# Optimization experiments

Hardware: AMD Instinct MI355X
Metric: run time of the kernel (lower is better)

## Reference

```python
import jax, jax.numpy as jnp
import numpy as np

BN_EPS = 1e-5


def setup_inputs() -> dict:
    key = jax.random.key(0)
    ks = jax.random.split(key, 8)
    B, S, D, H, O = 4, 25000, 128, 128, 128
    N, E = B * S, 600000
    x = jax.random.normal(ks[0], (B, S, D), dtype=jnp.float32)
    edge_index = jax.random.randint(ks[1], (2, E), 0, N)
    W1 = jax.random.normal(ks[2], (D, H), dtype=jnp.float32) * (1.0 / np.sqrt(D))
    b1 = jnp.zeros((H,), jnp.float32)
    gamma1 = jnp.ones((H,), jnp.float32)
    beta1 = jnp.zeros((H,), jnp.float32)
    W2 = jax.random.normal(ks[3], (H, O), dtype=jnp.float32) * (1.0 / np.sqrt(H))
    b2 = jnp.zeros((O,), jnp.float32)
    return {"x": x, "edge_index": edge_index, "W1": W1, "b1": b1,
            "gamma1": gamma1, "beta1": beta1, "W2": W2, "b2": b2}


def _gcn_norm(edge_index, num_nodes, dtype):
    # PyG gcn_norm: add self-loops, symmetric D^-1/2 (A+I) D^-1/2 edge weights.
    row, col = edge_index
    loop = jnp.arange(num_nodes, dtype=row.dtype)
    row_f = jnp.concatenate([row, loop])
    col_f = jnp.concatenate([col, loop])
    deg = jax.ops.segment_sum(jnp.ones(row_f.shape, dtype), row_f,
                              num_segments=num_nodes)
    dis = jnp.where(deg > 0, jax.lax.rsqrt(jnp.maximum(deg, 1e-12)), 0.0)
    norm = dis[row_f] * dis[col_f]  # [E + N]
    return row_f, col_f, norm


def _gcn_conv(h, W, b, row_f, col_f, norm, num_nodes):
    hw = h @ W                       # [N, out]
    msg = hw[col_f] * norm[:, None]  # gather + scale, [E+N, out]
    out = jax.ops.segment_sum(msg, row_f, num_segments=num_nodes)
    return out + b


def reference(x, edge_index, W1, b1, gamma1, beta1, W2, b2):
    B, S, D = x.shape
    N = B * S
    h = x.reshape(N, D)
    row_f, col_f, norm = _gcn_norm(edge_index, N, h.dtype)
    # layer 1: GCNConv -> BatchNorm (batch stats) -> ReLU (dropout inactive in eval)
    h = _gcn_conv(h, W1, b1, row_f, col_f, norm, N)
    mean = jnp.mean(h, axis=0)
    var = jnp.mean(jnp.square(h - mean), axis=0)
    h = gamma1 * (h - mean) * jax.lax.rsqrt(var + BN_EPS) + beta1
    h = jax.nn.relu(h)
    # layer 2: final GCNConv
    h = _gcn_conv(h, W2, b2, row_f, col_f, norm, N)
    return h.reshape(B, S, -1)
```

## Files before the change

kernel.cpp:

```cpp
#include <hip/hip_runtime.h>

#define DIM 128
#define BN_EPS 1e-5f
#define STAT_COPIES 64

typedef short short8 __attribute__((ext_vector_type(8)));
typedef float floatx4 __attribute__((ext_vector_type(4)));

__device__ __forceinline__ unsigned short f2bf(float f) {
    unsigned int u = __builtin_bit_cast(unsigned int, f);
    u += 0x7FFFu + ((u >> 16) & 1u);
    return (unsigned short)(u >> 16);
}
__device__ __forceinline__ float bf2f(unsigned short h) {
    return __builtin_bit_cast(float, (unsigned int)h << 16);
}


__global__ void deg_kernel(const int* __restrict__ row, int* __restrict__ deg, int E) {
    int e = blockIdx.x * blockDim.x + threadIdx.x;
    if (e < E) atomicAdd(&deg[row[e]], 1);
}


__global__ __launch_bounds__(256) void scan_block_kernel(const int* __restrict__ deg,
                                                         int* __restrict__ rowptr,
                                                         int* __restrict__ aux,
                                                         float* __restrict__ dis, int n) {
    __shared__ int ls[256];
    const int base = blockIdx.x * 1024;
    const int t = threadIdx.x;
    int v[4]; int s = 0;
    #pragma unroll
    for (int k = 0; k < 4; ++k) {
        int i = base + t * 4 + k;
        v[k] = (i < n) ? deg[i] : 0;
        s += v[k];
    }
    ls[t] = s;
    __syncthreads();
    for (int off = 1; off < 256; off <<= 1) {
        int x = (t >= off) ? ls[t - off] : 0;
        __syncthreads();
        ls[t] += x;
        __syncthreads();
    }
    int excl = ls[t] - s;
    if (t == 255) aux[blockIdx.x] = ls[255];
    #pragma unroll
    for (int k = 0; k < 4; ++k) {
        int i = base + t * 4 + k;
        if (i < n) {
            rowptr[i] = excl;
            dis[i] = rsqrtf((float)(v[k] + 1));
        }
        excl += v[k];
    }
}

__global__ __launch_bounds__(256) void scan_aux_kernel(int* __restrict__ aux, int nb,
                                                       int* __restrict__ rowptr, int n, int E) {
    __shared__ int ls[256];
    const int t = threadIdx.x;
    int v = (t < nb) ? aux[t] : 0;
    ls[t] = v;
    __syncthreads();
    for (int off = 1; off < 256; off <<= 1) {
        int x = (t >= off) ? ls[t - off] : 0;
        __syncthreads();
        ls[t] += x;
        __syncthreads();
    }
    if (t < nb) aux[t] = ls[t] - v;
    if (t == 0) rowptr[n] = E;
}

__global__ void add_offsets_kernel(int* __restrict__ rowptr, int* __restrict__ cursor,
                                   const int* __restrict__ aux, int n) {
    int i = blockIdx.x * blockDim.x + threadIdx.x;
    if (i < n) {
        int v = rowptr[i] + aux[i >> 10];
        rowptr[i] = v;
        cursor[i] = v;
    }
}


__global__ void scatter_kernel(const int* __restrict__ row, const int* __restrict__ col,
                               const float* __restrict__ dis, int* __restrict__ cursor,
                               int2* __restrict__ epack, int E) {
    int e = blockIdx.x * blockDim.x + threadIdx.x;
    if (e >= E) return;
    int r = row[e], c = col[e];
    int pos = atomicAdd(&cursor[r], 1);
    float nrm = dis[r] * dis[c];
    epack[pos] = make_int2(c, __builtin_bit_cast(int, nrm));
}


__global__ void convert_w_kernel(const float* __restrict__ W1, const float* __restrict__ W2,
                                 unsigned short* __restrict__ wfrag) {
    int s = blockIdx.x * blockDim.x + threadIdx.x;
    if (s >= 4096) return;
    int m  = s >> 11;
    int s2 = s & 2047;
    int kt = s2 >> 9;
    int nt = (s2 >> 6) & 7;
    int l  = s2 & 63;
    const float* W = m ? W2 : W1;
    unsigned short* o = wfrag + (size_t)m * 16384 + (size_t)s2 * 8;
    int k0 = kt * 32 + (l >> 4) * 8;
    int n0 = nt * 16 + (l & 15);
    #pragma unroll
    for (int j = 0; j < 8; ++j) o[j] = f2bf(W[(k0 + j) * DIM + n0]);
}


__global__ __launch_bounds__(256) void gemm_mfma_f32_kernel(
    const float* __restrict__ A, const unsigned short* __restrict__ wfrag,
    unsigned short* __restrict__ C, int n)
{
    __shared__ unsigned short sA[64][136];
    const int tid  = threadIdx.x;
    const int row0 = blockIdx.x * 64;

    #pragma unroll
    for (int l = 0; l < 8; ++l) {
        int idx = tid + l * 256;
        int r   = idx >> 5;
        int c4  = (idx & 31) * 4;
        float4 v;
        if (row0 + r < n) v = *(const float4*)(A + (size_t)(row0 + r) * DIM + c4);
        else              v = make_float4(0.f, 0.f, 0.f, 0.f);
        unsigned int lo = (unsigned int)f2bf(v.x) | ((unsigned int)f2bf(v.y) << 16);
        unsigned int hi = (unsigned int)f2bf(v.z) | ((unsigned int)f2bf(v.w) << 16);
        *(uint2*)(&sA[r][c4]) = make_uint2(lo, hi);
    }
    __syncthreads();

    const int wave = tid >> 6;
    const int lane = tid & 63;
    const int m    = lane & 15;
    const int quad = lane >> 4;
    const int rowA = wave * 16 + m;

    short8 af[4];
    #pragma unroll
    for (int kt = 0; kt < 4; ++kt)
        af[kt] = *(const short8*)(&sA[rowA][kt * 32 + quad * 8]);

    floatx4 acc[8];
    #pragma unroll
    for (int nt = 0; nt < 8; ++nt) acc[nt] = (floatx4){0.f, 0.f, 0.f, 0.f};

    #pragma unroll
    for (int nt = 0; nt < 8; ++nt)
        #pragma unroll
        for (int kt = 0; kt < 4; ++kt) {
            short8 bfr = *(const short8*)(wfrag + ((size_t)(kt * 8 + nt) * 64 + lane) * 8);
            acc[nt] = __builtin_amdgcn_mfma_f32_16x16x32_bf16(af[kt], bfr, acc[nt], 0, 0, 0);
        }

    #pragma unroll
    for (int nt = 0; nt < 8; ++nt)
        #pragma unroll
        for (int r = 0; r < 4; ++r) {
            int rr = row0 + wave * 16 + quad * 4 + r;
            if (rr < n) C[(size_t)rr * DIM + nt * 16 + m] = f2bf(acc[nt][r]);
        }
}


__global__ __launch_bounds__(256) void gemm_mfma_bn_kernel(
    const unsigned short* __restrict__ A, const unsigned short* __restrict__ wfrag,
    unsigned short* __restrict__ C, int n,
    const float* __restrict__ mean, const float* __restrict__ istd,
    const float* __restrict__ gamma, const float* __restrict__ beta)
{
    __shared__ unsigned short sA[64][136];
    const int tid  = threadIdx.x;
    const int row0 = blockIdx.x * 64;

    #pragma unroll
    for (int l = 0; l < 4; ++l) {
        int idx = tid + l * 256;
        int r   = idx >> 4;
        int c8  = (idx & 15) * 8;
        uint4 u = make_uint4(0, 0, 0, 0);
        if (row0 + r < n) u = *(const uint4*)(A + (size_t)(row0 + r) * DIM + c8);
        float f[8] = { bf2f((unsigned short)(u.x & 0xffff)), bf2f((unsigned short)(u.x >> 16)),
                       bf2f((unsigned short)(u.y & 0xffff)), bf2f((unsigned short)(u.y >> 16)),
                       bf2f((unsigned short)(u.z & 0xffff)), bf2f((unsigned short)(u.z >> 16)),
                       bf2f((unsigned short)(u.w & 0xffff)), bf2f((unsigned short)(u.w >> 16)) };
        #pragma unroll
        for (int k = 0; k < 8; ++k) {
            int c = c8 + k;
            f[k] = fmaxf(fmaf(gamma[c] * (f[k] - mean[c]), istd[c], beta[c]), 0.f);
        }
        uint4 o;
        o.x = (unsigned int)f2bf(f[0]) | ((unsigned int)f2bf(f[1]) << 16);
        o.y = (unsigned int)f2bf(f[2]) | ((unsigned int)f2bf(f[3]) << 16);
        o.z = (unsigned int)f2bf(f[4]) | ((unsigned int)f2bf(f[5]) << 16);
        o.w = (unsigned int)f2bf(f[6]) | ((unsigned int)f2bf(f[7]) << 16);
        *(uint4*)(&sA[r][c8]) = o;
    }
    __syncthreads();

    const int wave = tid >> 6;
    const int lane = tid & 63;
    const int m    = lane & 15;
    const int quad = lane >> 4;
    const int rowA = wave * 16 + m;

    short8 af[4];
    #pragma unroll
    for (int kt = 0; kt < 4; ++kt)
        af[kt] = *(const short8*)(&sA[rowA][kt * 32 + quad * 8]);

    floatx4 acc[8];
    #pragma unroll
    for (int nt = 0; nt < 8; ++nt) acc[nt] = (floatx4){0.f, 0.f, 0.f, 0.f};

    #pragma unroll
    for (int nt = 0; nt < 8; ++nt)
        #pragma unroll
        for (int kt = 0; kt < 4; ++kt) {
            short8 bfr = *(const short8*)(wfrag + ((size_t)(kt * 8 + nt) * 64 + lane) * 8);
            acc[nt] = __builtin_amdgcn_mfma_f32_16x16x32_bf16(af[kt], bfr, acc[nt], 0, 0, 0);
        }

    #pragma unroll
    for (int nt = 0; nt < 8; ++nt)
        #pragma unroll
        for (int r = 0; r < 4; ++r) {
            int rr = row0 + wave * 16 + quad * 4 + r;
            if (rr < n) C[(size_t)rr * DIM + nt * 16 + m] = f2bf(acc[nt][r]);
        }
}


__device__ __forceinline__ void acc8(float* acc, uint4 u, float w) {
    unsigned int a[4] = {u.x, u.y, u.z, u.w};
    #pragma unroll
    for (int k = 0; k < 4; ++k) {
        acc[2*k]   = fmaf(bf2f((unsigned short)(a[k] & 0xffff)), w, acc[2*k]);
        acc[2*k+1] = fmaf(bf2f((unsigned short)(a[k] >> 16)),    w, acc[2*k+1]);
    }
}

template <bool OUT_BF16, bool STATS>
__global__ __launch_bounds__(256) void agg_csr_kernel(
    const unsigned short* __restrict__ hw, const float* __restrict__ dis,
    const int* __restrict__ rowptr, const int2* __restrict__ epack,
    const float* __restrict__ bias, void* __restrict__ out_, int n,
    float* __restrict__ stat)
{
    const int sub  = threadIdx.x >> 4;
    const int l    = threadIdx.x & 15;
    const int node = blockIdx.x * 16 + sub;
    const bool valid = node < n;
    const int j = l * 8;

    float acc[8];
    #pragma unroll
    for (int k = 0; k < 8; ++k) acc[k] = 0.f;

    if (valid) {
        {
            const float d = dis[node];
            uint4 u = *(const uint4*)(hw + (size_t)node * DIM + j);
            acc8(acc, u, d * d);
        }

        int p  = rowptr[node];
        const int pe = rowptr[node + 1];
        for (; p + 3 < pe; p += 4) {
            int2 e0 = epack[p],     e1 = epack[p + 1];
            int2 e2 = epack[p + 2], e3 = epack[p + 3];
            uint4 u0 = *(const uint4*)(hw + (size_t)e0.x * DIM + j);
            uint4 u1 = *(const uint4*)(hw + (size_t)e1.x * DIM + j);
            uint4 u2 = *(const uint4*)(hw + (size_t)e2.x * DIM + j);
            uint4 u3 = *(const uint4*)(hw + (size_t)e3.x * DIM + j);
            acc8(acc, u0, __builtin_bit_cast(float, e0.y));
            acc8(acc, u1, __builtin_bit_cast(float, e1.y));
            acc8(acc, u2, __builtin_bit_cast(float, e2.y));
            acc8(acc, u3, __builtin_bit_cast(float, e3.y));
        }
        if (p + 1 < pe) {
            int2 e0 = epack[p], e1 = epack[p + 1];
            uint4 u0 = *(const uint4*)(hw + (size_t)e0.x * DIM + j);
            uint4 u1 = *(const uint4*)(hw + (size_t)e1.x * DIM + j);
            acc8(acc, u0, __builtin_bit_cast(float, e0.y));
            acc8(acc, u1, __builtin_bit_cast(float, e1.y));
            p += 2;
        }
        if (p < pe) {
            int2 e = epack[p];
            uint4 u = *(const uint4*)(hw + (size_t)e.x * DIM + j);
            acc8(acc, u, __builtin_bit_cast(float, e.y));
        }

        float4 b0 = *(const float4*)(bias + j);
        float4 b1 = *(const float4*)(bias + j + 4);
        acc[0] += b0.x; acc[1] += b0.y; acc[2] += b0.z; acc[3] += b0.w;
        acc[4] += b1.x; acc[5] += b1.y; acc[6] += b1.z; acc[7] += b1.w;

        if (OUT_BF16) {
            unsigned short* out = (unsigned short*)out_;
            uint4 o;
            o.x = (unsigned int)f2bf(acc[0]) | ((unsigned int)f2bf(acc[1]) << 16);
            o.y = (unsigned int)f2bf(acc[2]) | ((unsigned int)f2bf(acc[3]) << 16);
            o.z = (unsigned int)f2bf(acc[4]) | ((unsigned int)f2bf(acc[5]) << 16);
            o.w = (unsigned int)f2bf(acc[6]) | ((unsigned int)f2bf(acc[7]) << 16);
            *(uint4*)(out + (size_t)node * DIM + j) = o;
        } else {
            float* out = (float*)out_;
            *(float4*)(out + (size_t)node * DIM + j)     = make_float4(acc[0], acc[1], acc[2], acc[3]);
            *(float4*)(out + (size_t)node * DIM + j + 4) = make_float4(acc[4], acc[5], acc[6], acc[7]);
        }
    }

    if constexpr (STATS) {
        __shared__ float red[16][257];
        #pragma unroll
        for (int k = 0; k < 8; ++k) {
            float a = valid ? acc[k] : 0.f;
            red[sub][j + k]       = a;
            red[sub][128 + j + k] = a * a;
        }
        __syncthreads();
        float t = 0.f;
        #pragma unroll
        for (int r = 0; r < 16; ++r) t += red[r][threadIdx.x];
        atomicAdd(&stat[(blockIdx.x & (STAT_COPIES - 1)) * 256 + threadIdx.x], t);
    }
}

__global__ void bn_finalize_kernel(const float* __restrict__ stat, float* __restrict__ mi, int n) {
    int j = threadIdx.x;
    if (j < DIM) {
        float s = 0.f, q = 0.f;
        #pragma unroll 4
        for (int c = 0; c < STAT_COPIES; ++c) {
            s += stat[c * 256 + j];
            q += stat[c * 256 + 128 + j];
        }
        float mean = s / (float)n;
        float var  = q / (float)n - mean * mean;
        mi[j]       = mean;
        mi[DIM + j] = rsqrtf(var + BN_EPS);
    }
}


extern "C" void kernel_launch(void* const* d_in, const int* in_sizes, int n_in,
                              void* d_out, int out_size, void* d_ws, size_t ws_size,
                              hipStream_t stream)
{
    const float* x      = (const float*)d_in[0];
    const int*   ei     = (const int*)  d_in[1];
    const float* W1     = (const float*)d_in[2];
    const float* b1     = (const float*)d_in[3];
    const float* gamma1 = (const float*)d_in[4];
    const float* beta1  = (const float*)d_in[5];
    const float* W2     = (const float*)d_in[6];
    const float* b2     = (const float*)d_in[7];
    float* out = (float*)d_out;

    const int N = in_sizes[0] / DIM;
    const int E = in_sizes[1] / 2;
    const int* row = ei;
    const int* col = ei + E;

    const int NB = (N + 1023) / 1024;

    unsigned short* hw    = (unsigned short*)d_ws;
    unsigned short* h1    = hw + (size_t)N * DIM;
    int2*  epack  = (int2*)(h1 + (size_t)N * DIM);
    unsigned short* wfrag = (unsigned short*)(epack + E);
    float* dis    = (float*)(wfrag + 2 * 16384);
    int*   deg    = (int*)(dis + N);
    int*   cursor = deg + N;
    int*   rowptr = cursor + N;
    int*   aux    = rowptr + N + 1;
    float* stat   = (float*)(aux + 256);
    float* mi     = stat + STAT_COPIES * 256;

    hipMemsetAsync(deg,  0, (size_t)N * sizeof(int), stream);
    hipMemsetAsync(stat, 0, (size_t)STAT_COPIES * 256 * sizeof(float), stream);

    deg_kernel<<<(E + 255) / 256, 256, 0, stream>>>(row, deg, E);
    scan_block_kernel<<<NB, 256, 0, stream>>>(deg, rowptr, aux, dis, N);
    scan_aux_kernel<<<1, 256, 0, stream>>>(aux, NB, rowptr, N, E);
    add_offsets_kernel<<<(N + 255) / 256, 256, 0, stream>>>(rowptr, cursor, aux, N);
    scatter_kernel<<<(E + 255) / 256, 256, 0, stream>>>(row, col, dis, cursor, epack, E);
    convert_w_kernel<<<16, 256, 0, stream>>>(W1, W2, wfrag);

    gemm_mfma_f32_kernel<<<(N + 63) / 64, 256, 0, stream>>>(x, wfrag, hw, N);
    agg_csr_kernel<true, true><<<(N + 15) / 16, 256, 0, stream>>>(hw, dis, rowptr, epack,
                                                                  b1, h1, N, stat);
    bn_finalize_kernel<<<1, DIM, 0, stream>>>(stat, mi, N);

    gemm_mfma_bn_kernel<<<(N + 63) / 64, 256, 0, stream>>>(h1, wfrag + 16384, hw, N,
                                                           mi, mi + DIM, gamma1, beta1);
    agg_csr_kernel<false, false><<<(N + 15) / 16, 256, 0, stream>>>(hw, dis, rowptr, epack,
                                                                    b2, out, N, nullptr);
}
```

Before: 290.6 us.

## Merge preprocessing kernels, fold BN finalize into aggregation, batch edge gathers by eight

Cuts launches by co-scheduling independent work in shared grids: degree counting with weight conversion, and the CSR scatter with the first GEMM. The aux scan and BN finalize kernels are dropped. Each add_offsets block now reduces the preceding block sums itself, and the last aggregation block, found with a done-counter, computes BN scale and shift. The aggregation loop issues eight clamped edge loads and gathers at a time for more memory-level parallelism, and row bounds come packed as int2. Costs are redundant per-block reductions, clamped duplicate loads on short rows, and reliance on a threadfence/atomic last-block pattern for correctness.

```diff
diff --git a/kernel.cpp b/kernel.cpp
--- a/kernel.cpp
+++ b/kernel.cpp
@@ -17,9 +17,29 @@
 }
 
 
-__global__ void deg_kernel(const int* __restrict__ row, int* __restrict__ deg, int E) {
-    int e = blockIdx.x * blockDim.x + threadIdx.x;
-    if (e < E) atomicAdd(&deg[row[e]], 1);
+__global__ __launch_bounds__(256) void deg_convw_kernel(
+    const int* __restrict__ row, int* __restrict__ deg, int E, int degB,
+    const float* __restrict__ W1, const float* __restrict__ W2,
+    unsigned short* __restrict__ wfrag)
+{
+    if ((int)blockIdx.x < degB) {
+        int e = blockIdx.x * 256 + threadIdx.x;
+        if (e < E) atomicAdd(&deg[row[e]], 1);
+    } else {
+        int s = (blockIdx.x - degB) * 256 + threadIdx.x;
+        if (s >= 4096) return;
+        int m  = s >> 11;
+        int s2 = s & 2047;
+        int kt = s2 >> 9;
+        int nt = (s2 >> 6) & 7;
+        int l  = s2 & 63;
+        const float* W = m ? W2 : W1;
+        unsigned short* o = wfrag + (size_t)m * 16384 + (size_t)s2 * 8;
+        int k0 = kt * 32 + (l >> 4) * 8;
+        int n0 = nt * 16 + (l & 15);
+        #pragma unroll
+        for (int j = 0; j < 8; ++j) o[j] = f2bf(W[(k0 + j) * DIM + n0]);
+    }
 }
 
 
@@ -58,124 +78,104 @@
     }
 }
 
-__global__ __launch_bounds__(256) void scan_aux_kernel(int* __restrict__ aux, int nb,
-                                                       int* __restrict__ rowptr, int n, int E) {
-    __shared__ int ls[256];
+
+__global__ __launch_bounds__(256) void add_offsets_kernel(
+    const int* __restrict__ rowptr, const int* __restrict__ deg,
+    const int* __restrict__ aux, int2* __restrict__ rp2,
+    int* __restrict__ cursor, int n)
+{
+    __shared__ int red[256];
     const int t = threadIdx.x;
-    int v = (t < nb) ? aux[t] : 0;
-    ls[t] = v;
+    red[t] = (t < (int)blockIdx.x) ? aux[t] : 0;
     __syncthreads();
-    for (int off = 1; off < 256; off <<= 1) {
-        int x = (t >= off) ? ls[t - off] : 0;
-        __syncthreads();
-        ls[t] += x;
-        __syncthreads();
-    }
-    if (t < nb) aux[t] = ls[t] - v;
-    if (t == 0) rowptr[n] = E;
-}
-
-__global__ void add_offsets_kernel(int* __restrict__ rowptr, int* __restrict__ cursor,
-                                   const int* __restrict__ aux, int n) {
-    int i = blockIdx.x * blockDim.x + threadIdx.x;
-    if (i < n) {
-        int v = rowptr[i] + aux[i >> 10];
-        rowptr[i] = v;
-        cursor[i] = v;
-    }
-}
-
-
-__global__ void scatter_kernel(const int* __restrict__ row, const int* __restrict__ col,
-                               const float* __restrict__ dis, int* __restrict__ cursor,
-                               int2* __restrict__ epack, int E) {
-    int e = blockIdx.x * blockDim.x + threadIdx.x;
-    if (e >= E) return;
-    int r = row[e], c = col[e];
-    int pos = atomicAdd(&cursor[r], 1);
-    float nrm = dis[r] * dis[c];
-    epack[pos] = make_int2(c, __builtin_bit_cast(int, nrm));
-}
-
-
-__global__ void convert_w_kernel(const float* __restrict__ W1, const float* __restrict__ W2,
-                                 unsigned short* __restrict__ wfrag) {
-    int s = blockIdx.x * blockDim.x + threadIdx.x;
-    if (s >= 4096) return;
-    int m  = s >> 11;
-    int s2 = s & 2047;
-    int kt = s2 >> 9;
-    int nt = (s2 >> 6) & 7;
-    int l  = s2 & 63;
-    const float* W = m ? W2 : W1;
-    unsigned short* o = wfrag + (size_t)m * 16384 + (size_t)s2 * 8;
-    int k0 = kt * 32 + (l >> 4) * 8;
-    int n0 = nt * 16 + (l & 15);
-    #pragma unroll
-    for (int j = 0; j < 8; ++j) o[j] = f2bf(W[(k0 + j) * DIM + n0]);
-}
-
-
-__global__ __launch_bounds__(256) void gemm_mfma_f32_kernel(
+    for (int off = 128; off > 0; off >>= 1) {
+        if (t < off) red[t] += red[t + off];
+        __syncthreads();
+    }
+    const int base = red[0];
+    #pragma unroll
+    for (int k = 0; k < 4; ++k) {
+        int i = blockIdx.x * 1024 + t * 4 + k;
+        if (i < n) {
+            int st = rowptr[i] + base;
+            rp2[i] = make_int2(st, st + deg[i]);
+            cursor[i] = st;
+        }
+    }
+}
+
+
+__global__ __launch_bounds__(256) void scatter_gemm1_kernel(
+    const int* __restrict__ row, const int* __restrict__ col,
+    const float* __restrict__ dis, int* __restrict__ cursor,
+    int2* __restrict__ epack, int E, int scatB,
     const float* __restrict__ A, const unsigned short* __restrict__ wfrag,
     unsigned short* __restrict__ C, int n)
 {
-    __shared__ unsigned short sA[64][136];
-    const int tid  = threadIdx.x;
-    const int row0 = blockIdx.x * 64;
-
-    #pragma unroll
-    for (int l = 0; l < 8; ++l) {
-        int idx = tid + l * 256;
-        int r   = idx >> 5;
-        int c4  = (idx & 31) * 4;
-        float4 v;
-        if (row0 + r < n) v = *(const float4*)(A + (size_t)(row0 + r) * DIM + c4);
-        else              v = make_float4(0.f, 0.f, 0.f, 0.f);
-        unsigned int lo = (unsigned int)f2bf(v.x) | ((unsigned int)f2bf(v.y) << 16);
-        unsigned int hi = (unsigned int)f2bf(v.z) | ((unsigned int)f2bf(v.w) << 16);
-        *(uint2*)(&sA[r][c4]) = make_uint2(lo, hi);
-    }
-    __syncthreads();
-
-    const int wave = tid >> 6;
-    const int lane = tid & 63;
-    const int m    = lane & 15;
-    const int quad = lane >> 4;
-    const int rowA = wave * 16 + m;
-
-    short8 af[4];
-    #pragma unroll
-    for (int kt = 0; kt < 4; ++kt)
-        af[kt] = *(const short8*)(&sA[rowA][kt * 32 + quad * 8]);
-
-    floatx4 acc[8];
-    #pragma unroll
-    for (int nt = 0; nt < 8; ++nt) acc[nt] = (floatx4){0.f, 0.f, 0.f, 0.f};
-
-    #pragma unroll
-    for (int nt = 0; nt < 8; ++nt)
-        #pragma unroll
-        for (int kt = 0; kt < 4; ++kt) {
-            short8 bfr = *(const short8*)(wfrag + ((size_t)(kt * 8 + nt) * 64 + lane) * 8);
-            acc[nt] = __builtin_amdgcn_mfma_f32_16x16x32_bf16(af[kt], bfr, acc[nt], 0, 0, 0);
-        }
-
-    #pragma unroll
-    for (int nt = 0; nt < 8; ++nt)
-        #pragma unroll
-        for (int r = 0; r < 4; ++r) {
-            int rr = row0 + wave * 16 + quad * 4 + r;
-            if (rr < n) C[(size_t)rr * DIM + nt * 16 + m] = f2bf(acc[nt][r]);
-        }
+    if ((int)blockIdx.x < scatB) {
+        int e = blockIdx.x * 256 + threadIdx.x;
+        if (e >= E) return;
+        int r = row[e], c = col[e];
+        int pos = atomicAdd(&cursor[r], 1);
+        float nrm = dis[r] * dis[c];
+        epack[pos] = make_int2(c, __builtin_bit_cast(int, nrm));
+    } else {
+        __shared__ unsigned short sA[64][136];
+        const int tid  = threadIdx.x;
+        const int row0 = (blockIdx.x - scatB) * 64;
+
+        #pragma unroll
+        for (int l = 0; l < 8; ++l) {
+            int idx = tid + l * 256;
+            int r   = idx >> 5;
+            int c4  = (idx & 31) * 4;
+            float4 v;
+            if (row0 + r < n) v = *(const float4*)(A + (size_t)(row0 + r) * DIM + c4);
+            else              v = make_float4(0.f, 0.f, 0.f, 0.f);
+            unsigned int lo = (unsigned int)f2bf(v.x) | ((unsigned int)f2bf(v.y) << 16);
+            unsigned int hi = (unsigned int)f2bf(v.z) | ((unsigned int)f2bf(v.w) << 16);
+            *(uint2*)(&sA[r][c4]) = make_uint2(lo, hi);
+        }
+        __syncthreads();
+
+        const int wave = tid >> 6;
+        const int lane = tid & 63;
+        const int m    = lane & 15;
+        const int quad = lane >> 4;
+        const int rowA = wave * 16 + m;
+
+        short8 af[4];
+        #pragma unroll
+        for (int kt = 0; kt < 4; ++kt)
+            af[kt] = *(const short8*)(&sA[rowA][kt * 32 + quad * 8]);
+
+        floatx4 acc[8];
+        #pragma unroll
+        for (int nt = 0; nt < 8; ++nt) acc[nt] = (floatx4){0.f, 0.f, 0.f, 0.f};
+
+        #pragma unroll
+        for (int nt = 0; nt < 8; ++nt)
+            #pragma unroll
+            for (int kt = 0; kt < 4; ++kt) {
+                short8 bfr = *(const short8*)(wfrag + ((size_t)(kt * 8 + nt) * 64 + lane) * 8);
+                acc[nt] = __builtin_amdgcn_mfma_f32_16x16x32_bf16(af[kt], bfr, acc[nt], 0, 0, 0);
+            }
+
+        #pragma unroll
+        for (int nt = 0; nt < 8; ++nt)
+            #pragma unroll
+            for (int r = 0; r < 4; ++r) {
+                int rr = row0 + wave * 16 + quad * 4 + r;
+                if (rr < n) C[(size_t)rr * DIM + nt * 16 + m] = f2bf(acc[nt][r]);
+            }
+    }
 }
 
 
 __global__ __launch_bounds__(256) void gemm_mfma_bn_kernel(
     const unsigned short* __restrict__ A, const unsigned short* __restrict__ wfrag,
     unsigned short* __restrict__ C, int n,
-    const float* __restrict__ mean, const float* __restrict__ istd,
-    const float* __restrict__ gamma, const float* __restrict__ beta)
+    const float* __restrict__ mi)
 {
     __shared__ unsigned short sA[64][136];
     const int tid  = threadIdx.x;
@@ -195,7 +195,7 @@
         #pragma unroll
         for (int k = 0; k < 8; ++k) {
             int c = c8 + k;
-            f[k] = fmaxf(fmaf(gamma[c] * (f[k] - mean[c]), istd[c], beta[c]), 0.f);
+            f[k] = fmaxf(fmaf(f[k], mi[c], mi[128 + c]), 0.f);
         }
         uint4 o;
         o.x = (unsigned int)f2bf(f[0]) | ((unsigned int)f2bf(f[1]) << 16);
@@ -251,9 +251,11 @@
 template <bool OUT_BF16, bool STATS>
 __global__ __launch_bounds__(256) void agg_csr_kernel(
     const unsigned short* __restrict__ hw, const float* __restrict__ dis,
-    const int* __restrict__ rowptr, const int2* __restrict__ epack,
+    const int2* __restrict__ rp2, const int2* __restrict__ epack,
     const float* __restrict__ bias, void* __restrict__ out_, int n,
-    float* __restrict__ stat)
+    float* __restrict__ stat, unsigned int* __restrict__ donecnt,
+    const float* __restrict__ gamma, const float* __restrict__ beta,
+    float* __restrict__ mi)
 {
     const int sub  = threadIdx.x >> 4;
     const int l    = threadIdx.x & 15;
@@ -266,38 +268,31 @@
     for (int k = 0; k < 8; ++k) acc[k] = 0.f;
 
     if (valid) {
+        const int2 rp = rp2[node];
         {
             const float d = dis[node];
             uint4 u = *(const uint4*)(hw + (size_t)node * DIM + j);
             acc8(acc, u, d * d);
         }
 
-        int p  = rowptr[node];
-        const int pe = rowptr[node + 1];
-        for (; p + 3 < pe; p += 4) {
-            int2 e0 = epack[p],     e1 = epack[p + 1];
-            int2 e2 = epack[p + 2], e3 = epack[p + 3];
-            uint4 u0 = *(const uint4*)(hw + (size_t)e0.x * DIM + j);
-            uint4 u1 = *(const uint4*)(hw + (size_t)e1.x * DIM + j);
-            uint4 u2 = *(const uint4*)(hw + (size_t)e2.x * DIM + j);
-            uint4 u3 = *(const uint4*)(hw + (size_t)e3.x * DIM + j);
-            acc8(acc, u0, __builtin_bit_cast(float, e0.y));
-            acc8(acc, u1, __builtin_bit_cast(float, e1.y));
-            acc8(acc, u2, __builtin_bit_cast(float, e2.y));
-            acc8(acc, u3, __builtin_bit_cast(float, e3.y));
-        }
-        if (p + 1 < pe) {
-            int2 e0 = epack[p], e1 = epack[p + 1];
-            uint4 u0 = *(const uint4*)(hw + (size_t)e0.x * DIM + j);
-            uint4 u1 = *(const uint4*)(hw + (size_t)e1.x * DIM + j);
-            acc8(acc, u0, __builtin_bit_cast(float, e0.y));
-            acc8(acc, u1, __builtin_bit_cast(float, e1.y));
-            p += 2;
-        }
-        if (p < pe) {
-            int2 e = epack[p];
-            uint4 u = *(const uint4*)(hw + (size_t)e.x * DIM + j);
-            acc8(acc, u, __builtin_bit_cast(float, e.y));
+        const int pe = rp.y;
+        for (int p = rp.x; p < pe; p += 8) {
+            const int pm = pe - 1;
+            int2 e[8];
+            #pragma unroll
+            for (int k = 0; k < 8; ++k) {
+                int pk = p + k;
+                e[k] = epack[pk < pm ? pk : pm];
+            }
+            uint4 u[8];
+            #pragma unroll
+            for (int k = 0; k < 8; ++k)
+                u[k] = *(const uint4*)(hw + (size_t)e[k].x * DIM + j);
+            #pragma unroll
+            for (int k = 0; k < 8; ++k) {
+                float w = (p + k < pe) ? __builtin_bit_cast(float, e[k].y) : 0.f;
+                acc8(acc, u[k], w);
+            }
         }
 
         float4 b0 = *(const float4*)(bias + j);
@@ -322,6 +317,7 @@
 
     if constexpr (STATS) {
         __shared__ float red[16][257];
+        __shared__ int lastFlag;
         #pragma unroll
         for (int k = 0; k < 8; ++k) {
             float a = valid ? acc[k] : 0.f;
@@ -333,22 +329,29 @@
         #pragma unroll
         for (int r = 0; r < 16; ++r) t += red[r][threadIdx.x];
         atomicAdd(&stat[(blockIdx.x & (STAT_COPIES - 1)) * 256 + threadIdx.x], t);
-    }
-}
-
-__global__ void bn_finalize_kernel(const float* __restrict__ stat, float* __restrict__ mi, int n) {
-    int j = threadIdx.x;
-    if (j < DIM) {
-        float s = 0.f, q = 0.f;
-        #pragma unroll 4
-        for (int c = 0; c < STAT_COPIES; ++c) {
-            s += stat[c * 256 + j];
-            q += stat[c * 256 + 128 + j];
-        }
-        float mean = s / (float)n;
-        float var  = q / (float)n - mean * mean;
-        mi[j]       = mean;
-        mi[DIM + j] = rsqrtf(var + BN_EPS);
+
+        __threadfence();
+        if (threadIdx.x == 0) {
+            unsigned prev = atomicAdd(donecnt, 1u);
+            lastFlag = (prev == gridDim.x - 1) ? 1 : 0;
+        }
+        __syncthreads();
+        if (lastFlag && threadIdx.x < DIM) {
+            const int c = threadIdx.x;
+            float s = 0.f, q = 0.f;
+            for (int cp = 0; cp < STAT_COPIES; ++cp) {
+                s += __hip_atomic_load(&stat[cp * 256 + c],       __ATOMIC_RELAXED,
+                                       __HIP_MEMORY_SCOPE_AGENT);
+                q += __hip_atomic_load(&stat[cp * 256 + 128 + c], __ATOMIC_RELAXED,
+                                       __HIP_MEMORY_SCOPE_AGENT);
+            }
+            float mean  = s / (float)n;
+            float var   = q / (float)n - mean * mean;
+            float istd  = rsqrtf(var + BN_EPS);
+            float scale = gamma[c] * istd;
+            mi[c]       = scale;
+            mi[DIM + c] = fmaf(-mean, scale, beta[c]);
+        }
     }
 }
 
@@ -372,37 +375,37 @@
     const int* row = ei;
     const int* col = ei + E;
 
-    const int NB = (N + 1023) / 1024;
+    const int NB    = (N + 1023) / 1024;
+    const int degB  = (E + 255) / 256;
+    const int gemmB = (N + 63) / 64;
+    const int aggB  = (N + 15) / 16;
 
     unsigned short* hw    = (unsigned short*)d_ws;
     unsigned short* h1    = hw + (size_t)N * DIM;
     int2*  epack  = (int2*)(h1 + (size_t)N * DIM);
-    unsigned short* wfrag = (unsigned short*)(epack + E);
+    int2*  rp2    = epack + E;
+    unsigned short* wfrag = (unsigned short*)(rp2 + N);
     float* dis    = (float*)(wfrag + 2 * 16384);
-    int*   deg    = (int*)(dis + N);
-    int*   cursor = deg + N;
+    int*   cursor = (int*)(dis + N);
     int*   rowptr = cursor + N;
-    int*   aux    = rowptr + N + 1;
-    float* stat   = (float*)(aux + 256);
-    float* mi     = stat + STAT_COPIES * 256;
-
-    hipMemsetAsync(deg,  0, (size_t)N * sizeof(int), stream);
-    hipMemsetAsync(stat, 0, (size_t)STAT_COPIES * 256 * sizeof(float), stream);
-
-    deg_kernel<<<(E + 255) / 256, 256, 0, stream>>>(row, deg, E);
+    int*   aux    = rowptr + N;
+    float* mi     = (float*)(aux + 256);
+    int*   deg    = (int*)(mi + 256);
+    float* stat   = (float*)(deg + N);
+    unsigned int* donecnt = (unsigned int*)(stat + STAT_COPIES * 256);
+    const size_t zero_bytes = (size_t)N * 4 + (size_t)STAT_COPIES * 256 * 4 + 16;
+
+    hipMemsetAsync(deg, 0, zero_bytes, stream);
+
+    deg_convw_kernel<<<degB + 16, 256, 0, stream>>>(row, deg, E, degB, W1, W2, wfrag);
     scan_block_kernel<<<NB, 256, 0, stream>>>(deg, rowptr, aux, dis, N);
-    scan_aux_kernel<<<1, 256, 0, stream>>>(aux, NB, rowptr, N, E);
-    add_offsets_kernel<<<(N + 255) / 256, 256, 0, stream>>>(rowptr, cursor, aux, N);
-    scatter_kernel<<<(E + 255) / 256, 256, 0, stream>>>(row, col, dis, cursor, epack, E);
-    convert_w_kernel<<<16, 256, 0, stream>>>(W1, W2, wfrag);
-
-    gemm_mfma_f32_kernel<<<(N + 63) / 64, 256, 0, stream>>>(x, wfrag, hw, N);
-    agg_csr_kernel<true, true><<<(N + 15) / 16, 256, 0, stream>>>(hw, dis, rowptr, epack,
-                                                                  b1, h1, N, stat);
-    bn_finalize_kernel<<<1, DIM, 0, stream>>>(stat, mi, N);
-
-    gemm_mfma_bn_kernel<<<(N + 63) / 64, 256, 0, stream>>>(h1, wfrag + 16384, hw, N,
-                                                           mi, mi + DIM, gamma1, beta1);
-    agg_csr_kernel<false, false><<<(N + 15) / 16, 256, 0, stream>>>(hw, dis, rowptr, epack,
-                                                                    b2, out, N, nullptr);
-}
+    add_offsets_kernel<<<NB, 256, 0, stream>>>(rowptr, deg, aux, rp2, cursor, N);
+    scatter_gemm1_kernel<<<degB + gemmB, 256, 0, stream>>>(row, col, dis, cursor, epack,
+                                                           E, degB, x, wfrag, hw, N);
+    agg_csr_kernel<true, true><<<aggB, 256, 0, stream>>>(hw, dis, rp2, epack, b1, h1, N,
+                                                         stat, donecnt, gamma1, beta1, mi);
+    gemm_mfma_bn_kernel<<<gemmB, 256, 0, stream>>>(h1, wfrag + 16384, hw, N, mi);
+    agg_csr_kernel<false, false><<<aggB, 256, 0, stream>>>(hw, dis, rp2, epack, b2, out, N,
+                                                           nullptr, nullptr, nullptr, nullptr,
+                                                           nullptr);
+}
```

Measured after the change: 882.8 us. +203.8%, slower.
